# Optimization experiments

Hardware: AMD Instinct MI355X
Metric: run time of the kernel (lower is better)

Reference implementation:

```python
import jax, jax.numpy as jnp
import numpy as np

K_F = 3
NUM = K_F * K_F - 1      # 8 non-reference neighbors
IDX_REF = NUM // 2       # 4: reference pixel inserted in the middle
PROP_TIME = 18


def _conv2d(x, w, b, pad):
    y = jax.lax.conv_general_dilated(x, w, (1, 1), [(pad, pad), (pad, pad)],
                                     dimension_numbers=("NCHW", "OIHW", "NCHW"))
    return y + b[None, :, None, None]


def _offset_affinity(guidance, conv_w, conv_b, aff_scale):
    # TGASS branch of _get_offset_affinity
    B, _, H, W = guidance.shape
    pad_g = (conv_w.shape[2] - 1) // 2
    oa = _conv2d(guidance, conv_w, conv_b, pad_g)          # [B, 3*NUM, H, W]
    o1, o2, aff = jnp.split(oa, 3, axis=1)
    # torch: cat((o1,o2),1).view(B, NUM, 2, H, W) -- plain reinterpret of channels
    off = jnp.concatenate([o1, o2], axis=1).reshape(B, NUM, 2, H, W)
    zeros = jnp.zeros((B, 1, 2, H, W), off.dtype)
    off = jnp.concatenate([off[:, :IDX_REF], zeros, off[:, IDX_REF:]], axis=1)  # [B,9,2,H,W]
    aff = jnp.tanh(aff) / (aff_scale + 1e-8)               # TGASS scaling
    s = jnp.sum(jnp.abs(aff), axis=1, keepdims=True) + 1e-4
    s = jnp.maximum(s, 1.0)                                # aff_abs_sum[<1]=1
    aff = aff / s
    aff_ref = 1.0 - jnp.sum(aff, axis=1, keepdims=True)
    aff = jnp.concatenate([aff[:, :IDX_REF], aff_ref, aff[:, IDX_REF:]], axis=1)  # [B,9,H,W]
    return off.reshape(B, 2 * (NUM + 1), H, W), aff


def _bilinear(img, y, x):
    # img [B,H,W]; y,x [B,K,H,W] absolute sampling coords; zero outside (DCN zero padding)
    H, W = img.shape[1], img.shape[2]
    y0 = jnp.floor(y)
    x0 = jnp.floor(x)
    ty = y - y0
    tx = x - x0

    def g(yi, xi):
        valid = (yi >= 0) & (yi <= H - 1) & (xi >= 0) & (xi <= W - 1)
        yc = jnp.clip(yi, 0, H - 1).astype(jnp.int32)
        xc = jnp.clip(xi, 0, W - 1).astype(jnp.int32)
        v = jax.vmap(lambda im, a, b: im[a, b])(img, yc, xc)
        return jnp.where(valid, v, 0.0)

    return ((1 - ty) * (1 - tx) * g(y0, x0) + (1 - ty) * tx * g(y0, x0 + 1)
            + ty * (1 - tx) * g(y0 + 1, x0) + ty * tx * g(y0 + 1, x0 + 1))


def _nlspn_forward(feat_init, guidance, confidence, conv_w, conv_b, aff_scale):
    B, _, H, W = feat_init.shape
    dt = feat_init.dtype
    offset, aff = _offset_affinity(guidance, conv_w, conv_b, aff_scale)
    off = offset.reshape(B, NUM + 1, 2, H, W)
    off_y, off_x = off[:, :, 0], off[:, :, 1]              # [B,9,H,W]
    kk = jnp.arange(NUM + 1)
    grid_y = (kk // K_F - 1).astype(dt)[None, :, None, None]
    grid_x = (kk % K_F - 1).astype(dt)[None, :, None, None]
    base_y = jnp.arange(H, dtype=dt)[None, None, :, None]
    base_x = jnp.arange(W, dtype=dt)[None, None, None, :]
    # absolute sampling coordinates, constant across propagation steps
    yy = base_y + grid_y + off_y                           # [B,9,H,W]
    xx = base_x + grid_x + off_x

    def step(feat, _):
        # modulated deform conv with w==1, b==0, groups=1: weighted gather-sum
        s = _bilinear((feat * confidence)[:, 0], yy, xx)   # [B,9,H,W]
        nf = jnp.sum(aff * s, axis=1, keepdims=True)       # [B,1,H,W]
        return nf, nf

    feat_final, feats = jax.lax.scan(step, feat_init, None, length=PROP_TIME)
    return feat_final, feats, offset, aff, aff_scale


def setup_inputs() -> dict:
    key = jax.random.key(0)
    k1, k2, k3, k4 = jax.random.split(key, 4)
    B, CG, H, W = 4, 8, 240, 1216
    feat_init = jax.random.uniform(k1, (B, 1, H, W), dtype=jnp.float32)
    guidance = jax.random.normal(k2, (B, CG, H, W), dtype=jnp.float32)
    confidence = jax.random.uniform(k3, (B, 1, H, W), dtype=jnp.float32)
    conv_w = 0.1 * jax.random.normal(k4, (3 * NUM, CG, 3, 3), dtype=jnp.float32)
    conv_b = jnp.zeros((3 * NUM,), jnp.float32)
    aff_scale = jnp.full((1,), 0.5 * NUM, jnp.float32)     # affinity_gamma * num
    return {"feat_init": feat_init, "guidance": guidance, "confidence": confidence,
            "conv_w": conv_w, "conv_b": conv_b, "aff_scale": aff_scale}


def reference(feat_init, guidance, confidence, conv_w, conv_b, aff_scale):
    return _nlspn_forward(feat_init, guidance, confidence, conv_w, conv_b, aff_scale)
```

## Files before the change

### kernel.cpp

```cpp
#include <hip/hip_runtime.h>

#define BB 4
#define CG 8
#define HH 240
#define WW 1216
#define HW (HH*WW)
#define NPIX (BB*HW)

#define TW 128
#define TH 4
#define MG 8
#define LW (TW + 2*MG)
#define LH (TH + 2*MG)
#define NXT ((WW + TW - 1)/TW)
#define NYT (HH/TH)

struct __attribute__((packed, aligned(4))) Tap {
    unsigned pack;
    unsigned frac;
    float    av;
};

__global__ __launch_bounds__(256) void conv_fused(
    const float* __restrict__ g, const float* __restrict__ cw,
    const float* __restrict__ cb, const float* __restrict__ asc,
    const float* __restrict__ feat_init, const float* __restrict__ conf,
    float* __restrict__ out_off, float* __restrict__ out_aff,
    float* __restrict__ out_scale,
    Tap* __restrict__ tp, float* __restrict__ fc0)
{
    int gid = blockIdx.x * 256 + threadIdx.x;
    if (gid == 0) out_scale[0] = asc[0];
    if (gid >= NPIX) return;
    int w = gid % WW;
    int tmp = gid / WW;
    int h = tmp % HH;
    int b = tmp / HH;

    float acc[24];
    #pragma unroll
    for (int o = 0; o < 24; ++o) acc[o] = cb[o];

    const float* gb = g + (size_t)b * CG * HW;
    for (int i = 0; i < CG; ++i) {
        for (int kh = 0; kh < 3; ++kh) {
            int y = h + kh - 1;
            if ((unsigned)y >= (unsigned)HH) continue;
            for (int kw = 0; kw < 3; ++kw) {
                int x = w + kw - 1;
                if ((unsigned)x >= (unsigned)WW) continue;
                float xv = gb[i * HW + y * WW + x];
                #pragma unroll
                for (int o = 0; o < 24; ++o)
                    acc[o] = fmaf(xv, cw[((o * CG + i) * 3 + kh) * 3 + kw], acc[o]);
            }
        }
    }

    int pix = h * WW + w;

    float oyk[9], oxk[9];
    #pragma unroll
    for (int k = 0; k < 9; ++k) {
        if (k < 4)       { oyk[k] = acc[2 * k];     oxk[k] = acc[2 * k + 1]; }
        else if (k == 4) { oyk[k] = 0.0f;           oxk[k] = 0.0f; }
        else             { oyk[k] = acc[2 * k - 2]; oxk[k] = acc[2 * k - 1]; }
        out_off[(size_t)(b * 18 + 2 * k) * HW + pix]     = oyk[k];
        out_off[(size_t)(b * 18 + 2 * k + 1) * HW + pix] = oxk[k];
    }

    float inv = 1.0f / (asc[0] + 1e-8f);
    float a[8];
    float s = 0.0f;
    #pragma unroll
    for (int c = 0; c < 8; ++c) {
        a[c] = tanhf(acc[16 + c]) * inv;
        s += fabsf(a[c]);
    }
    s += 1e-4f;
    s = fmaxf(s, 1.0f);
    float sum = 0.0f;
    #pragma unroll
    for (int c = 0; c < 8; ++c) {
        a[c] = a[c] / s;
        sum += a[c];
    }
    float a9[9];
    #pragma unroll
    for (int c = 0; c < 4; ++c) a9[c] = a[c];
    a9[4] = 1.0f - sum;
    #pragma unroll
    for (int c = 4; c < 8; ++c) a9[c + 1] = a[c];

    #pragma unroll
    for (int k = 0; k < 9; ++k)
        out_aff[(size_t)(b * 9 + k) * HW + pix] = a9[k];

    if (tp) {
        #pragma unroll
        for (int k = 0; k < 9; ++k) {
            float yy = (float)(h + k / 3 - 1) + oyk[k];
            float xx = (float)(w + k % 3 - 1) + oxk[k];
            float y0f = floorf(yy), x0f = floorf(xx);
            float ty = yy - y0f, tx = xx - x0f;

            unsigned vy0 = (y0f >= 0.0f   && y0f <= 239.0f)  ? 1u : 0u;
            unsigned vy1 = (y0f >= -1.0f  && y0f <= 238.0f)  ? 1u : 0u;
            unsigned vx0 = (x0f >= 0.0f   && x0f <= 1215.0f) ? 1u : 0u;
            unsigned vx1 = (x0f >= -1.0f  && x0f <= 1214.0f) ? 1u : 0u;

            int y0i = (int)fminf(fmaxf(y0f, -1.0f), 239.0f);
            int x0i = (int)fminf(fmaxf(x0f, -1.0f), 1215.0f);

            unsigned pack = (unsigned)(y0i + 1) | ((unsigned)(x0i + 1) << 8)
                          | (vy0 << 19) | (vy1 << 20) | (vx0 << 21) | (vx1 << 22);
            unsigned tyq = (unsigned)(fminf(ty, 0.99999f) * 65535.0f + 0.5f);
            unsigned txq = (unsigned)(fminf(tx, 0.99999f) * 65535.0f + 0.5f);

            unsigned* t = (unsigned*)&tp[(size_t)k * NPIX + gid];
            t[0] = pack;
            t[1] = tyq | (txq << 16);
            t[2] = __float_as_uint(a9[k]);
        }
        fc0[gid] = feat_init[gid] * conf[gid];
    }
}

__global__ __launch_bounds__(512) void prop3(
    const float* __restrict__ fcIn, const float* __restrict__ conf,
    const Tap* __restrict__ tp,
    float* __restrict__ fout, float* __restrict__ fcOut, float* __restrict__ ffinal)
{
    __shared__ float sfc[LH * LW];

    int bx = blockIdx.x % NXT;
    int by = blockIdx.x / NXT;
    int b  = blockIdx.y;
    int xs = bx * TW, ys = by * TH;

    int rlo = max(0, ys - MG), rhi = min(HH - 1, ys + TH - 1 + MG);
    int clo = max(0, xs - MG), chi = min(WW - 1, xs + TW - 1 + MG);
    int rh = rhi - rlo + 1;

    const float* fcb = fcIn + (size_t)b * HW;

    for (int i = threadIdx.x; i < rh * LW; i += 512) {
        int r = i / LW;
        int c = i - r * LW;
        int col = min(clo + c, WW - 1);
        sfc[i] = fcb[(rlo + r) * WW + col];
    }
    __syncthreads();

    int tx = threadIdx.x & (TW - 1);
    int tyy = threadIdx.x >> 7;
    int x = xs + tx, y = ys + tyy;
    if (x >= WW) return;
    int pix = y * WW + x;
    int gid = b * HW + pix;

    float res = 0.0f;
    #pragma unroll
    for (int k = 0; k < 9; ++k) {
        const unsigned* tw = (const unsigned*)&tp[(size_t)k * NPIX + gid];
        unsigned Px = tw[0];
        unsigned Py = tw[1];
        float    av = __uint_as_float(tw[2]);

        int y0 = (int)(Px & 0xffu) - 1;
        int x0 = (int)((Px >> 8) & 0x7ffu) - 1;
        float ty = (float)(Py & 0xffffu) * (1.0f / 65535.0f);
        float txf = (float)(Py >> 16)    * (1.0f / 65535.0f);
        float fy0 = (Px & (1u << 19)) ? 1.0f : 0.0f;
        float fy1 = (Px & (1u << 20)) ? 1.0f : 0.0f;
        float fx0 = (Px & (1u << 21)) ? 1.0f : 0.0f;
        float fx1 = (Px & (1u << 22)) ? 1.0f : 0.0f;

        int yA = max(y0, 0), yB = min(y0 + 1, HH - 1);
        int xA = max(x0, 0), xB = min(x0 + 1, WW - 1);

        float v00, v01, v10, v11;
        if (yA >= rlo && yB <= rhi && xA >= clo && xB <= chi) {
            int rA = (yA - rlo) * LW - clo;
            int rB = (yB - rlo) * LW - clo;
            v00 = sfc[rA + xA]; v01 = sfc[rA + xB];
            v10 = sfc[rB + xA]; v11 = sfc[rB + xB];
        } else {
            int rA = yA * WW, rB = yB * WW;
            v00 = fcb[rA + xA]; v01 = fcb[rA + xB];
            v10 = fcb[rB + xA]; v11 = fcb[rB + xB];
        }

        float cy0 = fy0 * (1.0f - ty),  cy1 = fy1 * ty;
        float cx0 = fx0 * (1.0f - txf), cx1 = fx1 * txf;

        float u0 = fmaf(cx1, v01, cx0 * v00);
        float u1 = fmaf(cx1, v11, cx0 * v10);
        res = fmaf(av, fmaf(cy1, u1, cy0 * u0), res);
    }
    fout[gid] = res;
    if (fcOut)  fcOut[gid]  = res * conf[gid];
    if (ffinal) ffinal[gid] = res;
}

__device__ __forceinline__ float sampPC(const float* __restrict__ fb,
                                        const float* __restrict__ cf,
                                        int y, int x) {
    bool valid = ((unsigned)y < (unsigned)HH) && ((unsigned)x < (unsigned)WW);
    int yc = min(max(y, 0), HH - 1);
    int xc = min(max(x, 0), WW - 1);
    int idx = yc * WW + xc;
    float v = fb[idx] * cf[idx];
    return valid ? v : 0.0f;
}

__global__ __launch_bounds__(256) void prop(
    const float* __restrict__ fp, const float* __restrict__ conf,
    const float* __restrict__ off, const float* __restrict__ aff,
    float* __restrict__ fout, float* __restrict__ ffinal)
{
    int gid = blockIdx.x * 256 + threadIdx.x;
    if (gid >= NPIX) return;
    int w = gid % WW;
    int tmp = gid / WW;
    int h = tmp % HH;
    int b = tmp / HH;
    int pix = h * WW + w;

    const float* fb = fp + (size_t)b * HW;
    const float* cf = conf + (size_t)b * HW;

    float res = 0.0f;
    #pragma unroll
    for (int k = 0; k < 9; ++k) {
        float oy = off[(size_t)(b * 18 + 2 * k) * HW + pix];
        float ox = off[(size_t)(b * 18 + 2 * k + 1) * HW + pix];
        float av = aff[(size_t)(b * 9 + k) * HW + pix];

        float yy = (float)(h + k / 3 - 1) + oy;
        float xx = (float)(w + k % 3 - 1) + ox;

        float y0f = floorf(yy), x0f = floorf(xx);
        float ty = yy - y0f, tx = xx - x0f;
        int y0 = (int)y0f, x0 = (int)x0f;

        float v00 = sampPC(fb, cf, y0,     x0);
        float v01 = sampPC(fb, cf, y0,     x0 + 1);
        float v10 = sampPC(fb, cf, y0 + 1, x0);
        float v11 = sampPC(fb, cf, y0 + 1, x0 + 1);

        float sk = (1.0f - ty) * (1.0f - tx) * v00
                 + (1.0f - ty) * tx          * v01
                 + ty          * (1.0f - tx) * v10
                 + ty          * tx          * v11;
        res = fmaf(av, sk, res);
    }
    fout[gid] = res;
    if (ffinal) ffinal[gid] = res;
}

extern "C" void kernel_launch(void* const* d_in, const int* in_sizes, int n_in,
                              void* d_out, int out_size, void* d_ws, size_t ws_size,
                              hipStream_t stream) {
    const float* feat_init  = (const float*)d_in[0];
    const float* guidance   = (const float*)d_in[1];
    const float* confidence = (const float*)d_in[2];
    const float* conv_w     = (const float*)d_in[3];
    const float* conv_b     = (const float*)d_in[4];
    const float* aff_scale  = (const float*)d_in[5];

    float* out        = (float*)d_out;
    float* feat_final = out;
    float* feats      = out + (size_t)NPIX;
    float* offset     = out + (size_t)19 * NPIX;
    float* affout     = out + (size_t)37 * NPIX;
    float* scale_out  = out + (size_t)46 * NPIX;

    int nblocks = (NPIX + 255) / 256;

    size_t need = (size_t)9 * NPIX * 12 + (size_t)2 * NPIX * 4;

    if (ws_size >= need) {
        char* wsb = (char*)d_ws;
        Tap*   tpp = (Tap*)wsb;
        float* fcA = (float*)(wsb + (size_t)9 * NPIX * 12);
        float* fcB = fcA + NPIX;

        conv_fused<<<nblocks, 256, 0, stream>>>(guidance, conv_w, conv_b, aff_scale,
                                                feat_init, confidence,
                                                offset, affout, scale_out,
                                                tpp, fcA);

        dim3 pgrid(NXT * NYT, BB);
        float* fcIn = fcA;
        float* fcOut = fcB;
        for (int t = 0; t < 18; ++t) {
            float* cur = feats + (size_t)t * NPIX;
            prop3<<<pgrid, 512, 0, stream>>>(fcIn, confidence, tpp, cur,
                                             (t == 17) ? nullptr : fcOut,
                                             (t == 17) ? feat_final : nullptr);
            float* tmpp = fcIn; fcIn = fcOut; fcOut = tmpp;
        }
    } else {
        conv_fused<<<nblocks, 256, 0, stream>>>(guidance, conv_w, conv_b, aff_scale,
                                                feat_init, confidence,
                                                offset, affout, scale_out,
                                                nullptr, nullptr);
        const float* prev = feat_init;
        for (int t = 0; t < 18; ++t) {
            float* cur = feats + (size_t)t * NPIX;
            prop<<<nblocks, 256, 0, stream>>>(prev, confidence, offset, affout, cur,
                                              (t == 17) ? feat_final : nullptr);
            prev = cur;
        }
    }
}
```

Before: 714.7 us.

## Split tap table into 8-byte packed coords and affinity planes, skip center tap sampling

Replaces the packed 12-byte per-tap struct with an aligned 64-bit coordinate plane for the 8 non-reference taps plus a separate float affinity plane for all 9 taps. The center tap now reads the value straight from shared memory instead of doing a bilinear gather. This aims for wider aligned loads and less per-step work in the 18 propagation launches. Output writes use nontemporal stores to keep them from displacing reused data in cache. Total tap-table bytes per step are roughly the same, so any gain depends on better load vectorization.

```diff
diff --git a/kernel.cpp b/kernel.cpp
--- a/kernel.cpp
+++ b/kernel.cpp
@@ -15,19 +15,14 @@
 #define NXT ((WW + TW - 1)/TW)
 #define NYT (HH/TH)
 
-struct __attribute__((packed, aligned(4))) Tap {
-    unsigned pack;
-    unsigned frac;
-    float    av;
-};
-
 __global__ __launch_bounds__(256) void conv_fused(
     const float* __restrict__ g, const float* __restrict__ cw,
     const float* __restrict__ cb, const float* __restrict__ asc,
     const float* __restrict__ feat_init, const float* __restrict__ conf,
     float* __restrict__ out_off, float* __restrict__ out_aff,
     float* __restrict__ out_scale,
-    Tap* __restrict__ tp, float* __restrict__ fc0)
+    unsigned long long* __restrict__ paf, float* __restrict__ tav,
+    float* __restrict__ fc0)
 {
     int gid = blockIdx.x * 256 + threadIdx.x;
     if (gid == 0) out_scale[0] = asc[0];
@@ -65,8 +60,8 @@
         if (k < 4)       { oyk[k] = acc[2 * k];     oxk[k] = acc[2 * k + 1]; }
         else if (k == 4) { oyk[k] = 0.0f;           oxk[k] = 0.0f; }
         else             { oyk[k] = acc[2 * k - 2]; oxk[k] = acc[2 * k - 1]; }
-        out_off[(size_t)(b * 18 + 2 * k) * HW + pix]     = oyk[k];
-        out_off[(size_t)(b * 18 + 2 * k + 1) * HW + pix] = oxk[k];
+        __builtin_nontemporal_store(oyk[k], &out_off[(size_t)(b * 18 + 2 * k) * HW + pix]);
+        __builtin_nontemporal_store(oxk[k], &out_off[(size_t)(b * 18 + 2 * k + 1) * HW + pix]);
     }
 
     float inv = 1.0f / (asc[0] + 1e-8f);
@@ -94,11 +89,15 @@
 
     #pragma unroll
     for (int k = 0; k < 9; ++k)
-        out_aff[(size_t)(b * 9 + k) * HW + pix] = a9[k];
-
-    if (tp) {
+        __builtin_nontemporal_store(a9[k], &out_aff[(size_t)(b * 9 + k) * HW + pix]);
+
+    if (paf) {
         #pragma unroll
         for (int k = 0; k < 9; ++k) {
+            tav[(size_t)k * NPIX + gid] = a9[k];
+            if (k == 4) continue;
+            int j = (k < 4) ? k : k - 1;
+
             float yy = (float)(h + k / 3 - 1) + oyk[k];
             float xx = (float)(w + k % 3 - 1) + oxk[k];
             float y0f = floorf(yy), x0f = floorf(xx);
@@ -116,19 +115,18 @@
                           | (vy0 << 19) | (vy1 << 20) | (vx0 << 21) | (vx1 << 22);
             unsigned tyq = (unsigned)(fminf(ty, 0.99999f) * 65535.0f + 0.5f);
             unsigned txq = (unsigned)(fminf(tx, 0.99999f) * 65535.0f + 0.5f);
-
-            unsigned* t = (unsigned*)&tp[(size_t)k * NPIX + gid];
-            t[0] = pack;
-            t[1] = tyq | (txq << 16);
-            t[2] = __float_as_uint(a9[k]);
+            unsigned frac = tyq | (txq << 16);
+
+            paf[(size_t)j * NPIX + gid] =
+                (unsigned long long)pack | ((unsigned long long)frac << 32);
         }
         fc0[gid] = feat_init[gid] * conf[gid];
     }
 }
 
-__global__ __launch_bounds__(512) void prop3(
+__global__ __launch_bounds__(512) void prop4(
     const float* __restrict__ fcIn, const float* __restrict__ conf,
-    const Tap* __restrict__ tp,
+    const unsigned long long* __restrict__ paf, const float* __restrict__ tav,
     float* __restrict__ fout, float* __restrict__ fcOut, float* __restrict__ ffinal)
 {
     __shared__ float sfc[LH * LW];
@@ -159,13 +157,17 @@
     int pix = y * WW + x;
     int gid = b * HW + pix;
 
-    float res = 0.0f;
-    #pragma unroll
-    for (int k = 0; k < 9; ++k) {
-        const unsigned* tw = (const unsigned*)&tp[(size_t)k * NPIX + gid];
-        unsigned Px = tw[0];
-        unsigned Py = tw[1];
-        float    av = __uint_as_float(tw[2]);
+    float res = tav[(size_t)4 * NPIX + gid] *
+                sfc[(y - rlo) * LW + (x - clo)];
+
+    #pragma unroll
+    for (int j = 0; j < 8; ++j) {
+        int k = (j < 4) ? j : j + 1;
+        unsigned long long pf = paf[(size_t)j * NPIX + gid];
+        float av = tav[(size_t)k * NPIX + gid];
+
+        unsigned Px = (unsigned)pf;
+        unsigned Py = (unsigned)(pf >> 32);
 
         int y0 = (int)(Px & 0xffu) - 1;
         int x0 = (int)((Px >> 8) & 0x7ffu) - 1;
@@ -198,9 +200,9 @@
         float u1 = fmaf(cx1, v11, cx0 * v10);
         res = fmaf(av, fmaf(cy1, u1, cy0 * u0), res);
     }
-    fout[gid] = res;
-    if (fcOut)  fcOut[gid]  = res * conf[gid];
-    if (ffinal) ffinal[gid] = res;
+    __builtin_nontemporal_store(res, &fout[gid]);
+    if (fcOut)  fcOut[gid] = res * conf[gid];
+    if (ffinal) __builtin_nontemporal_store(res, &ffinal[gid]);
 }
 
 __device__ __forceinline__ float sampPC(const float* __restrict__ fb,
@@ -278,25 +280,26 @@
 
     int nblocks = (NPIX + 255) / 256;
 
-    size_t need = (size_t)9 * NPIX * 12 + (size_t)2 * NPIX * 4;
+    size_t need = (size_t)8 * NPIX * 8 + (size_t)9 * NPIX * 4 + (size_t)2 * NPIX * 4;
 
     if (ws_size >= need) {
         char* wsb = (char*)d_ws;
-        Tap*   tpp = (Tap*)wsb;
-        float* fcA = (float*)(wsb + (size_t)9 * NPIX * 12);
+        unsigned long long* paf = (unsigned long long*)wsb;
+        float* tav = (float*)(wsb + (size_t)8 * NPIX * 8);
+        float* fcA = (float*)(wsb + (size_t)8 * NPIX * 8 + (size_t)9 * NPIX * 4);
         float* fcB = fcA + NPIX;
 
         conv_fused<<<nblocks, 256, 0, stream>>>(guidance, conv_w, conv_b, aff_scale,
                                                 feat_init, confidence,
                                                 offset, affout, scale_out,
-                                                tpp, fcA);
+                                                paf, tav, fcA);
 
         dim3 pgrid(NXT * NYT, BB);
         float* fcIn = fcA;
         float* fcOut = fcB;
         for (int t = 0; t < 18; ++t) {
             float* cur = feats + (size_t)t * NPIX;
-            prop3<<<pgrid, 512, 0, stream>>>(fcIn, confidence, tpp, cur,
+            prop4<<<pgrid, 512, 0, stream>>>(fcIn, confidence, paf, tav, cur,
                                              (t == 17) ? nullptr : fcOut,
                                              (t == 17) ? feat_final : nullptr);
             float* tmpp = fcIn; fcIn = fcOut; fcOut = tmpp;
@@ -305,7 +308,7 @@
         conv_fused<<<nblocks, 256, 0, stream>>>(guidance, conv_w, conv_b, aff_scale,
                                                 feat_init, confidence,
                                                 offset, affout, scale_out,
-                                                nullptr, nullptr);
+                                                nullptr, nullptr, nullptr);
         const float* prev = feat_init;
         for (int t = 0; t < 18; ++t) {
             float* cur = feats + (size_t)t * NPIX;
```

Result: faster. 630.7 us (-11.7%).
